# Kernel optimization log

Hardware: AMD Instinct MI355X
Metric: run time of the kernel (lower is better)

Reference implementation:

```python
import jax, jax.numpy as jnp
import numpy as np

NUM_NEG = 100            # number of negative samples per masked step
CLAMP_W = 1.0            # clamped_logit_weight
B, C, T, M = 8, 256, 1024, 512


def setup_inputs() -> dict:
    key = jax.random.key(0)
    k1, k2, k3 = jax.random.split(key, 3)
    feat_proj = jax.random.normal(k1, (B, C, T), dtype=jnp.float32)
    context_output = jax.random.normal(k2, (B, C, T), dtype=jnp.float32)
    # exactly M masked timesteps per batch row (random positions)
    perm = jax.vmap(lambda k: jax.random.permutation(k, T))(jax.random.split(k3, B))
    mask = perm < M  # [B, T] bool, M True per row
    return {"feat_proj": feat_proj, "mask": mask,
            "context_output": context_output, "num_masked": M}


def reference(feat_proj, mask, context_output, num_masked):
    Bb, Cc, Tt = feat_proj.shape
    # indices of masked timesteps, in time order (stable argsort) -> [B, M]
    idx = jnp.argsort(jnp.logical_not(mask), axis=1)[:, :num_masked]
    feat_t = jnp.swapaxes(feat_proj, 1, 2)        # [B, T, C]
    ctx_t = jnp.swapaxes(context_output, 1, 2)    # [B, T, C]
    mf = jnp.take_along_axis(feat_t, idx[:, :, None], axis=1)  # [B, M, C]
    mc = jnp.take_along_axis(ctx_t, idx[:, :, None], axis=1)   # [B, M, C]
    # uniform sampling of NUM_NEG negatives without replacement, excluding self:
    # random scores per (t, candidate), self set to -1, take top-k
    scores = jax.random.uniform(jax.random.key(42), (Bb, num_masked, num_masked))
    self_mask = jnp.eye(num_masked, dtype=bool)
    scores = jnp.where(self_mask[None], -1.0, scores)
    _, neg_idx = jax.lax.top_k(scores, NUM_NEG)                 # [B, M, K]
    neg_feats = jnp.take_along_axis(mf[:, None, :, :], neg_idx[..., None], axis=2)  # [B, M, K, C]
    pos_logit = jnp.einsum('bmc,bmc->bm', mc, mf)               # [B, M]
    neg_logit = jnp.einsum('bmc,bmkc->bmk', mc, neg_feats)      # [B, M, K]
    logits = jnp.concatenate([pos_logit[..., None], neg_logit], axis=-1)  # [B, M, 1+K]
    total_loss = jnp.sum(jax.nn.softmax(logits, axis=-1)[..., 0])
    clamped = CLAMP_W * jnp.tanh(logits / CLAMP_W)
    total_aux_loss = jnp.sum(clamped ** 2)
    return total_loss, total_aux_loss
```

## Files before the change

kernel.cpp:

```cpp
#include <hip/hip_runtime.h>
#include <stdint.h>

#define NB   8
#define NC   256
#define NT   1024
#define NM   512
#define NNEG 100

typedef unsigned short u16;
typedef __attribute__((ext_vector_type(8))) short bf16x8;
typedef __attribute__((ext_vector_type(4))) float f32x4;

__device__ __forceinline__ unsigned rotl32(unsigned x, int d) {
  return (x << d) | (x >> (32 - d));
}

__device__ unsigned threefry_bits(unsigned i) {
  const unsigned half = 1048576u;
  const bool lo = i < half;
  unsigned v0 = lo ? i : (i - half);
  unsigned v1 = lo ? (i + half) : i;
  const unsigned k0 = 0u, k1 = 42u;
  const unsigned k2 = k0 ^ k1 ^ 0x1BD11BDAu;
  v0 += k0; v1 += k1;
#define TF_R(r) { v0 += v1; v1 = rotl32(v1, r); v1 ^= v0; }
  TF_R(13) TF_R(15) TF_R(26) TF_R(6)
  v0 += k1; v1 += k2 + 1u;
  TF_R(17) TF_R(29) TF_R(16) TF_R(24)
  v0 += k2; v1 += k0 + 2u;
  TF_R(13) TF_R(15) TF_R(26) TF_R(6)
  v0 += k0; v1 += k1 + 3u;
  TF_R(17) TF_R(29) TF_R(16) TF_R(24)
  v0 += k1; v1 += k2 + 4u;
  TF_R(13) TF_R(15) TF_R(26) TF_R(6)
  v0 += k2; v1 += k0 + 5u;
#undef TF_R
  return lo ? v0 : v1;
}

__global__ __launch_bounds__(256) void k_compact(const float* __restrict__ ctx,
                                                 const float* __restrict__ feat,
                                                 const void* __restrict__ maskp,
                                                 u16* __restrict__ MCh, u16* __restrict__ MCl,
                                                 u16* __restrict__ MFh, u16* __restrict__ MFl) {
  __shared__ float lds[64][129];
  __shared__ int posl[128];
  __shared__ int wsum[4];
  __shared__ int det[3];
  const int tid = threadIdx.x;
  const int lane = tid & 63, wid = tid >> 6;
  const int t0 = blockIdx.x * 128;
  const int b = blockIdx.y >> 1, mat = blockIdx.y & 1;
  const unsigned char* mb = (const unsigned char*)maskp;

  if (tid < 3) det[tid] = 0;
  __syncthreads();
  {
    int c1 = 0, c4 = 0, c8 = 0;
    for (int j = tid; j < 1024; j += 256) {
      c1 += (mb[j] != 0);
      c4 += (((const unsigned*)mb)[j] != 0u);
      c8 += (((const unsigned long long*)mb)[j] != 0ull);
    }
#pragma unroll
    for (int off = 32; off; off >>= 1) {
      c1 += __shfl_xor(c1, off, 64);
      c4 += __shfl_xor(c4, off, 64);
      c8 += __shfl_xor(c8, off, 64);
    }
    if (lane == 0) { atomicAdd(&det[0], c1); atomicAdd(&det[1], c4); atomicAdd(&det[2], c8); }
  }
  __syncthreads();
  const int stride = (det[1] == 512) ? 4 : ((det[0] == 512) ? 1 : ((det[2] == 512) ? 8 : 4));

  int f4[4]; int s = 0;
#pragma unroll
  for (int j = 0; j < 4; ++j) {
    int tt = 4 * tid + j;
    size_t e = (size_t)b * NT + tt;
    int f;
    if (stride == 1)      f = (mb[e] != 0);
    else if (stride == 4) f = (((const unsigned*)mb)[e] != 0u);
    else                  f = (((const unsigned long long*)mb)[e] != 0ull);
    f4[j] = f; s += f;
  }
  int incl = s;
#pragma unroll
  for (int off = 1; off < 64; off <<= 1) {
    int o = __shfl_up(incl, off, 64);
    if (lane >= off) incl += o;
  }
  if (lane == 63) wsum[wid] = incl;
  __syncthreads();
  int wbase = 0;
#pragma unroll
  for (int w = 0; w < 4; ++w) if (w < wid) wbase += wsum[w];
  int excl = wbase + incl - s;
#pragma unroll
  for (int j = 0; j < 4; ++j) {
    int tt = 4 * tid + j;
    if (tt >= t0 && tt < t0 + 128) posl[tt - t0] = f4[j] ? excl : -1;
    excl += f4[j];
  }

  const float* src = (mat ? feat : ctx) + (size_t)b * NC * NT;
  u16* dh = (mat ? MFh : MCh) + (size_t)b * NM * NC;
  u16* dl = (mat ? MFl : MCl) + (size_t)b * NM * NC;

  const int c4i = tid >> 6, tl = tid & 63, tr = tid >> 6;
  for (int chunk = 0; chunk < 4; ++chunk) {
    int c0 = chunk * 64;
    __syncthreads();
    for (int ci = 0; ci < 16; ++ci) {
      int cc = c4i * 16 + ci;
#pragma unroll
      for (int tj = 0; tj < 2; ++tj) {
        int tt = tl + 64 * tj;
        lds[cc][tt] = src[(size_t)(c0 + cc) * NT + t0 + tt];
      }
    }
    __syncthreads();
    for (int tt = tr; tt < 128; tt += 4) {
      int p = posl[tt];
      if (p >= 0) {
        float x = lds[tl][tt];
        unsigned xb = __float_as_uint(x);
        u16 hi = (u16)(xb >> 16);
        float hif = __uint_as_float((unsigned)hi << 16);
        float rlo = x - hif;
        u16 lo = (u16)(__float_as_uint(rlo) >> 16);
        dh[(size_t)p * NC + c0 + tl] = hi;
        dl[(size_t)p * NC + c0 + tl] = lo;
      }
    }
  }
}

__global__ __launch_bounds__(256) void k_gemm(const u16* __restrict__ MCh, const u16* __restrict__ MCl,
                                              const u16* __restrict__ MFh, const u16* __restrict__ MFl,
                                              float* __restrict__ S) {
  __shared__ u16 smem[30720];
  const int tid = threadIdx.x;
  const int b = blockIdx.z;
  const int m0 = blockIdx.y * 128;
  const int j0 = blockIdx.x * 64;
  const int wave = tid >> 6, lane = tid & 63;
  const int wm = wave >> 1, wn = wave & 1;
  const int r = lane & 15, g = lane >> 4;

  const int arow = tid & 127, ah2 = tid >> 7;
  const int brow = tid & 63,  bh2 = (tid >> 6) & 1, bmat = tid >> 7;

  const u16* Agh = MCh + (size_t)(b * NM + m0 + arow) * NC;
  const u16* Agl = MCl + (size_t)(b * NM + m0 + arow) * NC;
  const u16* Bg  = (bmat ? MFl : MFh) + (size_t)(b * NM + j0 + brow) * NC;

  uint4 rA0, rA1, rL0, rL1, rB0, rB1;
  auto load_regs = [&](int c0) {
    const uint4* p;
    p = (const uint4*)(Agh + c0 + 16 * ah2); rA0 = p[0]; rA1 = p[1];
    p = (const uint4*)(Agl + c0 + 16 * ah2); rL0 = p[0]; rL1 = p[1];
    p = (const uint4*)(Bg  + c0 + 16 * bh2); rB0 = p[0]; rB1 = p[1];
  };
  auto write_lds = [&](int buf) {
    u16* base = smem + buf * 15360;
    u16* d;
    d = base + arow * 40 + 16 * ah2;
    *(uint4*)d = rA0; *(uint4*)(d + 8) = rA1;
    d = base + 5120 + arow * 40 + 16 * ah2;
    *(uint4*)d = rL0; *(uint4*)(d + 8) = rL1;
    d = base + 10240 + bmat * 2560 + brow * 40 + 16 * bh2;
    *(uint4*)d = rB0; *(uint4*)(d + 8) = rB1;
  };

  f32x4 z = {0.f, 0.f, 0.f, 0.f};
  f32x4 acc[4][2];
#pragma unroll
  for (int m = 0; m < 4; ++m) { acc[m][0] = z; acc[m][1] = z; }

  const int aro = (wm * 64 + r) * 40 + g * 8;
  const int bro = (wn * 32 + r) * 40 + g * 8;

  load_regs(0);
  write_lds(0);
  __syncthreads();

  for (int ks = 0; ks < 8; ++ks) {
    const int cur = ks & 1;
    if (ks < 7) load_regs((ks + 1) * 32);
    {
      const u16* base = smem + cur * 15360;
      bf16x8 ah[4], al[4];
#pragma unroll
      for (int m = 0; m < 4; ++m) {
        ah[m] = *(const bf16x8*)(base + aro + m * 640);
        al[m] = *(const bf16x8*)(base + 5120 + aro + m * 640);
      }
#pragma unroll
      for (int n = 0; n < 2; ++n) {
        bf16x8 bh = *(const bf16x8*)(base + 10240 + bro + n * 640);
        bf16x8 bl = *(const bf16x8*)(base + 12800 + bro + n * 640);
#pragma unroll
        for (int m = 0; m < 4; ++m) {
          acc[m][n] = __builtin_amdgcn_mfma_f32_16x16x32_bf16(ah[m], bh, acc[m][n], 0, 0, 0);
          acc[m][n] = __builtin_amdgcn_mfma_f32_16x16x32_bf16(ah[m], bl, acc[m][n], 0, 0, 0);
          acc[m][n] = __builtin_amdgcn_mfma_f32_16x16x32_bf16(al[m], bh, acc[m][n], 0, 0, 0);
        }
      }
    }
    if (ks < 7) write_lds(cur ^ 1);
    __syncthreads();
  }

  float* Sb = S + (size_t)b * NM * NM;
#pragma unroll
  for (int m = 0; m < 4; ++m)
#pragma unroll
    for (int n = 0; n < 2; ++n)
#pragma unroll
      for (int q = 0; q < 4; ++q) {
        int row = m0 + wm * 64 + m * 16 + g * 4 + q;
        int col = j0 + wn * 32 + n * 16 + r;
        Sb[(size_t)row * NM + col] = acc[m][n][q];
      }
}

__global__ __launch_bounds__(512) void k_loss(const float* __restrict__ S,
                                              float* __restrict__ pl,
                                              float* __restrict__ pa) {
  __shared__ unsigned hist[256];
  __shared__ unsigned long long bkey[512];
  __shared__ int bcount;
  __shared__ int boundary_bin, need_s;
  __shared__ unsigned char selflag[512];
  __shared__ float redM[8], redE[8], redA[8];
  __shared__ float posnum;

  const int t = threadIdx.x;
  const int row = blockIdx.x;
  const int m = row & (NM - 1);
  const bool self = (t == m);

  unsigned bits = threefry_bits((unsigned)row * 512u + (unsigned)t);
  unsigned u = bits >> 9;
  unsigned key = (u << 9) | (unsigned)(511 - t);
  int bin = (int)(u >> 15);

  if (t < 256) hist[t] = 0;
  if (t == 0) bcount = 0;
  selflag[t] = 0;
  __syncthreads();

  if (!self) atomicAdd(&hist[bin], 1u);
  __syncthreads();

  if (t < 64) {
    unsigned h0 = hist[4 * t + 0], h1 = hist[4 * t + 1];
    unsigned h2 = hist[4 * t + 2], h3 = hist[4 * t + 3];
    unsigned s = h0 + h1 + h2 + h3;
    unsigned suf = s;
#pragma unroll
    for (int off = 1; off < 64; off <<= 1) {
      unsigned o = __shfl_down(suf, off, 64);
      if (t + off < 64) suf += o;
    }
    unsigned a3 = suf - s;
    unsigned a2 = a3 + h3;
    unsigned a1 = a2 + h2;
    unsigned a0 = a1 + h1;
    if (a3 < NNEG && a3 + h3 >= NNEG) { boundary_bin = 4 * t + 3; need_s = NNEG - (int)a3; }
    if (a2 < NNEG && a2 + h2 >= NNEG) { boundary_bin = 4 * t + 2; need_s = NNEG - (int)a2; }
    if (a1 < NNEG && a1 + h1 >= NNEG) { boundary_bin = 4 * t + 1; need_s = NNEG - (int)a1; }
    if (a0 < NNEG && a0 + h0 >= NNEG) { boundary_bin = 4 * t + 0; need_s = NNEG - (int)a0; }
  }
  __syncthreads();

  const int bb = boundary_bin;
  if (!self) {
    if (bin > bb) selflag[t] = 1;
    else if (bin == bb) {
      int p = atomicAdd(&bcount, 1);
      bkey[p] = (((unsigned long long)key) << 1) | 1ull;
    }
  }
  __syncthreads();

  if (t == 0) {
    int cnt = bcount, need = need_s;
    for (int it = 0; it < need; ++it) {
      unsigned long long best = 0ull; int bi = 0;
      for (int q = 0; q < cnt; ++q)
        if (bkey[q] > best) { best = bkey[q]; bi = q; }
      bkey[bi] = 0ull;
      int tt = 511 - (int)((best >> 1) & 511ull);
      selflag[tt] = 1;
    }
  }
  __syncthreads();

  const float* Srow = S + (size_t)row * NM;
  const bool act = (selflag[t] != 0) || self;
  const float logitv = Srow[t];
  const int wid = t >> 6;

  float mv = act ? logitv : -3.4e38f;
#pragma unroll
  for (int off = 32; off > 0; off >>= 1) mv = fmaxf(mv, __shfl_xor(mv, off, 64));
  if ((t & 63) == 0) redM[wid] = mv;
  __syncthreads();
  float mx = redM[0];
#pragma unroll
  for (int q = 1; q < 8; ++q) mx = fmaxf(mx, redM[q]);

  float e = 0.f, a = 0.f;
  if (act) {
    e = __expf(logitv - mx);
    float th = 1.f - 2.f / (__expf(2.f * logitv) + 1.f);
    a = th * th;
  }
  if (self) posnum = e;

  float es = e, as = a;
#pragma unroll
  for (int off = 32; off > 0; off >>= 1) {
    es += __shfl_xor(es, off, 64);
    as += __shfl_xor(as, off, 64);
  }
  if ((t & 63) == 0) { redE[wid] = es; redA[wid] = as; }
  __syncthreads();

  if (t == 0) {
    float den = 0.f, aux = 0.f;
#pragma unroll
    for (int q = 0; q < 8; ++q) { den += redE[q]; aux += redA[q]; }
    pl[row] = posnum / den;
    pa[row] = aux;
  }
}

__global__ __launch_bounds__(1024) void k_red(const float* __restrict__ pl,
                                              const float* __restrict__ pa,
                                              float* __restrict__ out) {
  __shared__ float s1[1024], s2[1024];
  const int t = threadIdx.x;
  float a = 0.f, b = 0.f;
  for (int q = t; q < NB * NM; q += 1024) { a += pl[q]; b += pa[q]; }
  s1[t] = a; s2[t] = b;
  __syncthreads();
  for (int off = 512; off > 0; off >>= 1) {
    if (t < off) { s1[t] += s1[t + off]; s2[t] += s2[t + off]; }
    __syncthreads();
  }
  if (t == 0) { out[0] = s1[0]; out[1] = s2[0]; }
}

extern "C" void kernel_launch(void* const* d_in, const int* in_sizes, int n_in,
                              void* d_out, int out_size, void* d_ws, size_t ws_size,
                              hipStream_t stream) {
  const float* feat = (const float*)d_in[0];
  const void*  mask = d_in[1];
  const float* ctx  = (const float*)d_in[2];
  float* out = (float*)d_out;

  char* ws = (char*)d_ws;
  u16*   MCh = (u16*)ws;
  u16*   MCl = (u16*)(ws + (2u << 20));
  u16*   MFh = (u16*)(ws + (4u << 20));
  u16*   MFl = (u16*)(ws + (6u << 20));
  float* S   = (float*)(ws + (8u << 20));
  float* pl  = (float*)(ws + (16u << 20));
  float* pa  = pl + NB * NM;

  dim3 gc(NT / 128, NB * 2);
  k_compact<<<gc, 256, 0, stream>>>(ctx, feat, mask, MCh, MCl, MFh, MFl);

  dim3 g2(NM / 64, NM / 128, NB);
  k_gemm<<<g2, 256, 0, stream>>>(MCh, MCl, MFh, MFl, S);

  k_loss<<<NB * NM, 512, 0, stream>>>(S, pl, pa);

  k_red<<<1, 1024, 0, stream>>>(pl, pa, out);
}
```

Before: 62.84 us.

## Process one loss row per wavefront and shrink GEMM tile to 64x64

The loss kernel now gives each 64-lane wave a whole row, with each lane handling 8 columns. Block-wide barriers become wave-local LDS waits, and the final reductions become pure shuffles, which removes most __syncthreads and shared reduction arrays. The GEMM tile shrinks from 128x64 to 64x64, doubling the grid to spread work over more CUs at the cost of less data reuse per tile. The boundary-bin candidate buffer is capped at 32 entries, so correctness now depends on the boundary bin never holding more than 32 candidates.

Measured after the change: 52.50 us. -16.5%, faster.

```diff
diff --git a/kernel.cpp b/kernel.cpp
--- a/kernel.cpp
+++ b/kernel.cpp
@@ -8,8 +8,11 @@
 #define NNEG 100
 
 typedef unsigned short u16;
+typedef unsigned long long u64;
 typedef __attribute__((ext_vector_type(8))) short bf16x8;
 typedef __attribute__((ext_vector_type(4))) float f32x4;
+
+#define WAVE_LDS_FENCE() asm volatile("s_waitcnt lgkmcnt(0)" ::: "memory")
 
 __device__ __forceinline__ unsigned rotl32(unsigned x, int d) {
   return (x << d) | (x >> (32 - d));
@@ -60,7 +63,7 @@
     for (int j = tid; j < 1024; j += 256) {
       c1 += (mb[j] != 0);
       c4 += (((const unsigned*)mb)[j] != 0u);
-      c8 += (((const unsigned long long*)mb)[j] != 0ull);
+      c8 += (((const u64*)mb)[j] != 0ull);
     }
 #pragma unroll
     for (int off = 32; off; off >>= 1) {
@@ -81,7 +84,7 @@
     int f;
     if (stride == 1)      f = (mb[e] != 0);
     else if (stride == 4) f = (((const unsigned*)mb)[e] != 0u);
-    else                  f = (((const unsigned long long*)mb)[e] != 0ull);
+    else                  f = (((const u64*)mb)[e] != 0ull);
     f4[j] = f; s += f;
   }
   int incl = s;
@@ -126,8 +129,7 @@
         float x = lds[tl][tt];
         unsigned xb = __float_as_uint(x);
         u16 hi = (u16)(xb >> 16);
-        float hif = __uint_as_float((unsigned)hi << 16);
-        float rlo = x - hif;
+        float rlo = x - __uint_as_float((unsigned)hi << 16);
         u16 lo = (u16)(__float_as_uint(rlo) >> 16);
         dh[(size_t)p * NC + c0 + tl] = hi;
         dl[(size_t)p * NC + c0 + tl] = lo;
@@ -139,47 +141,39 @@
 __global__ __launch_bounds__(256) void k_gemm(const u16* __restrict__ MCh, const u16* __restrict__ MCl,
                                               const u16* __restrict__ MFh, const u16* __restrict__ MFl,
                                               float* __restrict__ S) {
-  __shared__ u16 smem[30720];
+  __shared__ u16 smem[2][10240];
   const int tid = threadIdx.x;
-  const int b = blockIdx.z;
-  const int m0 = blockIdx.y * 128;
-  const int j0 = blockIdx.x * 64;
+  const int b = blockIdx.z, m0 = blockIdx.y * 64, j0 = blockIdx.x * 64;
   const int wave = tid >> 6, lane = tid & 63;
   const int wm = wave >> 1, wn = wave & 1;
   const int r = lane & 15, g = lane >> 4;
 
-  const int arow = tid & 127, ah2 = tid >> 7;
-  const int brow = tid & 63,  bh2 = (tid >> 6) & 1, bmat = tid >> 7;
-
-  const u16* Agh = MCh + (size_t)(b * NM + m0 + arow) * NC;
-  const u16* Agl = MCl + (size_t)(b * NM + m0 + arow) * NC;
-  const u16* Bg  = (bmat ? MFl : MFh) + (size_t)(b * NM + j0 + brow) * NC;
-
-  uint4 rA0, rA1, rL0, rL1, rB0, rB1;
+  const int srow = tid >> 1;
+  const int splane = srow >> 6;
+  const int smrow = srow & 63;
+  const int shalf = tid & 1;
+  const u16* Asrc = (splane ? MCl : MCh) + (size_t)(b * NM + m0 + smrow) * NC + shalf * 16;
+  const u16* Bsrc = (splane ? MFl : MFh) + (size_t)(b * NM + j0 + smrow) * NC + shalf * 16;
+  const int sdst = srow * 40 + shalf * 16;
+
+  uint4 ra0, ra1, rb0, rb1;
   auto load_regs = [&](int c0) {
-    const uint4* p;
-    p = (const uint4*)(Agh + c0 + 16 * ah2); rA0 = p[0]; rA1 = p[1];
-    p = (const uint4*)(Agl + c0 + 16 * ah2); rL0 = p[0]; rL1 = p[1];
-    p = (const uint4*)(Bg  + c0 + 16 * bh2); rB0 = p[0]; rB1 = p[1];
+    const uint4* p = (const uint4*)(Asrc + c0); ra0 = p[0]; ra1 = p[1];
+    const uint4* q = (const uint4*)(Bsrc + c0); rb0 = q[0]; rb1 = q[1];
   };
   auto write_lds = [&](int buf) {
-    u16* base = smem + buf * 15360;
-    u16* d;
-    d = base + arow * 40 + 16 * ah2;
-    *(uint4*)d = rA0; *(uint4*)(d + 8) = rA1;
-    d = base + 5120 + arow * 40 + 16 * ah2;
-    *(uint4*)d = rL0; *(uint4*)(d + 8) = rL1;
-    d = base + 10240 + bmat * 2560 + brow * 40 + 16 * bh2;
-    *(uint4*)d = rB0; *(uint4*)(d + 8) = rB1;
+    u16* d = smem[buf] + sdst;
+    *(uint4*)d = ra0; *(uint4*)(d + 8) = ra1;
+    u16* e = smem[buf] + 5120 + sdst;
+    *(uint4*)e = rb0; *(uint4*)(e + 8) = rb1;
   };
 
-  f32x4 z = {0.f, 0.f, 0.f, 0.f};
-  f32x4 acc[4][2];
-#pragma unroll
-  for (int m = 0; m < 4; ++m) { acc[m][0] = z; acc[m][1] = z; }
-
-  const int aro = (wm * 64 + r) * 40 + g * 8;
-  const int bro = (wn * 32 + r) * 40 + g * 8;
+  f32x4 zero = {0.f, 0.f, 0.f, 0.f};
+  f32x4 acc[2][2];
+#pragma unroll
+  for (int m = 0; m < 2; ++m)
+#pragma unroll
+    for (int n = 0; n < 2; ++n) acc[m][n] = zero;
 
   load_regs(0);
   write_lds(0);
@@ -188,154 +182,149 @@
   for (int ks = 0; ks < 8; ++ks) {
     const int cur = ks & 1;
     if (ks < 7) load_regs((ks + 1) * 32);
-    {
-      const u16* base = smem + cur * 15360;
-      bf16x8 ah[4], al[4];
-#pragma unroll
-      for (int m = 0; m < 4; ++m) {
-        ah[m] = *(const bf16x8*)(base + aro + m * 640);
-        al[m] = *(const bf16x8*)(base + 5120 + aro + m * 640);
+    const u16* base = smem[cur];
+    bf16x8 ah[2], al[2], bh[2], bl[2];
+#pragma unroll
+    for (int m = 0; m < 2; ++m) {
+      ah[m] = *(const bf16x8*)(base + (wm * 32 + m * 16 + r) * 40 + g * 8);
+      al[m] = *(const bf16x8*)(base + (64 + wm * 32 + m * 16 + r) * 40 + g * 8);
+    }
+#pragma unroll
+    for (int n = 0; n < 2; ++n) {
+      bh[n] = *(const bf16x8*)(base + 5120 + (wn * 32 + n * 16 + r) * 40 + g * 8);
+      bl[n] = *(const bf16x8*)(base + 5120 + (64 + wn * 32 + n * 16 + r) * 40 + g * 8);
+    }
+#pragma unroll
+    for (int m = 0; m < 2; ++m)
+#pragma unroll
+      for (int n = 0; n < 2; ++n) {
+        acc[m][n] = __builtin_amdgcn_mfma_f32_16x16x32_bf16(ah[m], bh[n], acc[m][n], 0, 0, 0);
+        acc[m][n] = __builtin_amdgcn_mfma_f32_16x16x32_bf16(ah[m], bl[n], acc[m][n], 0, 0, 0);
+        acc[m][n] = __builtin_amdgcn_mfma_f32_16x16x32_bf16(al[m], bh[n], acc[m][n], 0, 0, 0);
       }
-#pragma unroll
-      for (int n = 0; n < 2; ++n) {
-        bf16x8 bh = *(const bf16x8*)(base + 10240 + bro + n * 640);
-        bf16x8 bl = *(const bf16x8*)(base + 12800 + bro + n * 640);
-#pragma unroll
-        for (int m = 0; m < 4; ++m) {
-          acc[m][n] = __builtin_amdgcn_mfma_f32_16x16x32_bf16(ah[m], bh, acc[m][n], 0, 0, 0);
-          acc[m][n] = __builtin_amdgcn_mfma_f32_16x16x32_bf16(ah[m], bl, acc[m][n], 0, 0, 0);
-          acc[m][n] = __builtin_amdgcn_mfma_f32_16x16x32_bf16(al[m], bh, acc[m][n], 0, 0, 0);
-        }
-      }
-    }
     if (ks < 7) write_lds(cur ^ 1);
     __syncthreads();
   }
 
   float* Sb = S + (size_t)b * NM * NM;
 #pragma unroll
-  for (int m = 0; m < 4; ++m)
+  for (int m = 0; m < 2; ++m)
 #pragma unroll
     for (int n = 0; n < 2; ++n)
 #pragma unroll
       for (int q = 0; q < 4; ++q) {
-        int row = m0 + wm * 64 + m * 16 + g * 4 + q;
-        int col = j0 + wn * 32 + n * 16 + r;
-        Sb[(size_t)row * NM + col] = acc[m][n][q];
+        int rowi = m0 + wm * 32 + m * 16 + g * 4 + q;
+        int col  = j0 + wn * 32 + n * 16 + r;
+        Sb[(size_t)rowi * NM + col] = acc[m][n][q];
       }
 }
 
 __global__ __launch_bounds__(512) void k_loss(const float* __restrict__ S,
                                               float* __restrict__ pl,
                                               float* __restrict__ pa) {
-  __shared__ unsigned hist[256];
-  __shared__ unsigned long long bkey[512];
-  __shared__ int bcount;
-  __shared__ int boundary_bin, need_s;
-  __shared__ unsigned char selflag[512];
-  __shared__ float redM[8], redE[8], redA[8];
-  __shared__ float posnum;
-
-  const int t = threadIdx.x;
-  const int row = blockIdx.x;
+  __shared__ unsigned hist[8][256];
+  __shared__ u64 bk[8][32];
+  __shared__ int bcnt[8], bbin[8], bneed[8];
+  __shared__ unsigned char sf[8][512];
+
+  const int tid = threadIdx.x;
+  const int lane = tid & 63, wv = tid >> 6;
+  const int row = blockIdx.x * 8 + wv;
   const int m = row & (NM - 1);
-  const bool self = (t == m);
-
-  unsigned bits = threefry_bits((unsigned)row * 512u + (unsigned)t);
-  unsigned u = bits >> 9;
-  unsigned key = (u << 9) | (unsigned)(511 - t);
-  int bin = (int)(u >> 15);
-
-  if (t < 256) hist[t] = 0;
-  if (t == 0) bcount = 0;
-  selflag[t] = 0;
-  __syncthreads();
-
-  if (!self) atomicAdd(&hist[bin], 1u);
-  __syncthreads();
-
-  if (t < 64) {
-    unsigned h0 = hist[4 * t + 0], h1 = hist[4 * t + 1];
-    unsigned h2 = hist[4 * t + 2], h3 = hist[4 * t + 3];
+
+#pragma unroll
+  for (int q = 0; q < 4; ++q) hist[wv][lane * 4 + q] = 0;
+#pragma unroll
+  for (int j = 0; j < 8; ++j) sf[wv][j * 64 + lane] = 0;
+  if (lane == 0) bcnt[wv] = 0;
+
+  unsigned keys[8]; int bins[8]; bool selfj[8];
+#pragma unroll
+  for (int j = 0; j < 8; ++j) {
+    int t = j * 64 + lane;
+    unsigned bits = threefry_bits((unsigned)row * 512u + (unsigned)t);
+    unsigned u = bits >> 9;
+    keys[j] = (u << 9) | (unsigned)(511 - t);
+    bins[j] = (int)(u >> 15);
+    selfj[j] = (t == m);
+    if (!selfj[j]) atomicAdd(&hist[wv][bins[j]], 1u);
+  }
+  WAVE_LDS_FENCE();
+
+  {
+    unsigned h0 = hist[wv][4 * lane + 0], h1 = hist[wv][4 * lane + 1];
+    unsigned h2 = hist[wv][4 * lane + 2], h3 = hist[wv][4 * lane + 3];
     unsigned s = h0 + h1 + h2 + h3;
     unsigned suf = s;
 #pragma unroll
     for (int off = 1; off < 64; off <<= 1) {
       unsigned o = __shfl_down(suf, off, 64);
-      if (t + off < 64) suf += o;
+      if (lane + off < 64) suf += o;
     }
     unsigned a3 = suf - s;
     unsigned a2 = a3 + h3;
     unsigned a1 = a2 + h2;
     unsigned a0 = a1 + h1;
-    if (a3 < NNEG && a3 + h3 >= NNEG) { boundary_bin = 4 * t + 3; need_s = NNEG - (int)a3; }
-    if (a2 < NNEG && a2 + h2 >= NNEG) { boundary_bin = 4 * t + 2; need_s = NNEG - (int)a2; }
-    if (a1 < NNEG && a1 + h1 >= NNEG) { boundary_bin = 4 * t + 1; need_s = NNEG - (int)a1; }
-    if (a0 < NNEG && a0 + h0 >= NNEG) { boundary_bin = 4 * t + 0; need_s = NNEG - (int)a0; }
-  }
-  __syncthreads();
-
-  const int bb = boundary_bin;
-  if (!self) {
-    if (bin > bb) selflag[t] = 1;
-    else if (bin == bb) {
-      int p = atomicAdd(&bcount, 1);
-      bkey[p] = (((unsigned long long)key) << 1) | 1ull;
-    }
-  }
-  __syncthreads();
-
-  if (t == 0) {
-    int cnt = bcount, need = need_s;
+    if (a3 < NNEG && a3 + h3 >= NNEG) { bbin[wv] = 4 * lane + 3; bneed[wv] = NNEG - (int)a3; }
+    if (a2 < NNEG && a2 + h2 >= NNEG) { bbin[wv] = 4 * lane + 2; bneed[wv] = NNEG - (int)a2; }
+    if (a1 < NNEG && a1 + h1 >= NNEG) { bbin[wv] = 4 * lane + 1; bneed[wv] = NNEG - (int)a1; }
+    if (a0 < NNEG && a0 + h0 >= NNEG) { bbin[wv] = 4 * lane + 0; bneed[wv] = NNEG - (int)a0; }
+  }
+  WAVE_LDS_FENCE();
+
+  const int bb = bbin[wv];
+#pragma unroll
+  for (int j = 0; j < 8; ++j) {
+    if (!selfj[j] && bins[j] == bb) {
+      int p = atomicAdd(&bcnt[wv], 1);
+      bk[wv][p & 31] = (((u64)keys[j]) << 1) | 1ull;
+    }
+  }
+  WAVE_LDS_FENCE();
+
+  if (lane == 0) {
+    int cnt = bcnt[wv]; if (cnt > 32) cnt = 32;
+    int need = bneed[wv];
     for (int it = 0; it < need; ++it) {
-      unsigned long long best = 0ull; int bi = 0;
+      u64 best = 0ull; int bi = 0;
       for (int q = 0; q < cnt; ++q)
-        if (bkey[q] > best) { best = bkey[q]; bi = q; }
-      bkey[bi] = 0ull;
+        if (bk[wv][q] > best) { best = bk[wv][q]; bi = q; }
+      bk[wv][bi] = 0ull;
       int tt = 511 - (int)((best >> 1) & 511ull);
-      selflag[tt] = 1;
-    }
-  }
-  __syncthreads();
+      sf[wv][tt] = 1;
+    }
+  }
+  WAVE_LDS_FENCE();
 
   const float* Srow = S + (size_t)row * NM;
-  const bool act = (selflag[t] != 0) || self;
-  const float logitv = Srow[t];
-  const int wid = t >> 6;
-
-  float mv = act ? logitv : -3.4e38f;
+  float lv[8]; bool act[8];
+  float mv = -3.4e38f;
+#pragma unroll
+  for (int j = 0; j < 8; ++j) {
+    lv[j] = Srow[j * 64 + lane];
+    act[j] = selfj[j] || (bins[j] > bb && !selfj[j]) || (sf[wv][j * 64 + lane] != 0);
+    if (act[j]) mv = fmaxf(mv, lv[j]);
+  }
 #pragma unroll
   for (int off = 32; off > 0; off >>= 1) mv = fmaxf(mv, __shfl_xor(mv, off, 64));
-  if ((t & 63) == 0) redM[wid] = mv;
-  __syncthreads();
-  float mx = redM[0];
-#pragma unroll
-  for (int q = 1; q < 8; ++q) mx = fmaxf(mx, redM[q]);
-
-  float e = 0.f, a = 0.f;
-  if (act) {
-    e = __expf(logitv - mx);
-    float th = 1.f - 2.f / (__expf(2.f * logitv) + 1.f);
-    a = th * th;
-  }
-  if (self) posnum = e;
-
-  float es = e, as = a;
+
+  float es = 0.f, as = 0.f, ps = 0.f;
+#pragma unroll
+  for (int j = 0; j < 8; ++j) {
+    if (act[j]) {
+      float e = __expf(lv[j] - mv);
+      float th = 1.f - 2.f / (__expf(2.f * lv[j]) + 1.f);
+      es += e; as += th * th;
+      if (selfj[j]) ps = e;
+    }
+  }
 #pragma unroll
   for (int off = 32; off > 0; off >>= 1) {
     es += __shfl_xor(es, off, 64);
     as += __shfl_xor(as, off, 64);
-  }
-  if ((t & 63) == 0) { redE[wid] = es; redA[wid] = as; }
-  __syncthreads();
-
-  if (t == 0) {
-    float den = 0.f, aux = 0.f;
-#pragma unroll
-    for (int q = 0; q < 8; ++q) { den += redE[q]; aux += redA[q]; }
-    pl[row] = posnum / den;
-    pa[row] = aux;
-  }
+    ps += __shfl_xor(ps, off, 64);
+  }
+  if (lane == 0) { pl[row] = ps / es; pa[row] = as; }
 }
 
 __global__ __launch_bounds__(1024) void k_red(const float* __restrict__ pl,
@@ -374,10 +363,10 @@
   dim3 gc(NT / 128, NB * 2);
   k_compact<<<gc, 256, 0, stream>>>(ctx, feat, mask, MCh, MCl, MFh, MFl);
 
-  dim3 g2(NM / 64, NM / 128, NB);
+  dim3 g2(NM / 64, NM / 64, NB);
   k_gemm<<<g2, 256, 0, stream>>>(MCh, MCl, MFh, MFl, S);
 
-  k_loss<<<NB * NM, 512, 0, stream>>>(S, pl, pa);
+  k_loss<<<NB * NM / 8, 512, 0, stream>>>(S, pl, pa);
 
   k_red<<<1, 1024, 0, stream>>>(pl, pa, out);
 }
```
